# Kernel tuning notes

Hardware: AMD Instinct MI355X
Metric: run time of the kernel (lower is better)

The kernel has to match this reference:

```python
import jax, jax.numpy as jnp
import numpy as np

B, T, I, H, O = 64, 512, 64, 1024, 64
STEPS = 49 - 1  # output_len - 1 decode iterations


def _cell(x_t, h, c, Wih, Whh, b):
    # PyTorch LSTM gate order: i, f, g, o
    gates = x_t @ Wih.T + h @ Whh.T + b  # [B, 4H]
    i, f, g, o = jnp.split(gates, 4, axis=-1)
    i = jax.nn.sigmoid(i)
    f = jax.nn.sigmoid(f)
    g = jnp.tanh(g)
    o = jax.nn.sigmoid(o)
    c2 = f * c + i * g
    h2 = o * jnp.tanh(c2)
    return h2, c2


def setup_inputs() -> dict:
    key = jax.random.key(0)
    ks = jax.random.split(key, 12)
    s = 0.05
    return {
        "x": jax.random.normal(ks[0], (B, T, I), jnp.float32),
        "y0": jax.random.normal(ks[1], (B, I), jnp.float32),
        "Wih_e": jax.random.normal(ks[2], (4 * H, I), jnp.float32) * s,
        "Whh_e": jax.random.normal(ks[3], (4 * H, H), jnp.float32) * s,
        "bih_e": jax.random.normal(ks[4], (4 * H,), jnp.float32) * s,
        "bhh_e": jax.random.normal(ks[5], (4 * H,), jnp.float32) * s,
        "Wih_d": jax.random.normal(ks[6], (4 * H, I), jnp.float32) * s,
        "Whh_d": jax.random.normal(ks[7], (4 * H, H), jnp.float32) * s,
        "bih_d": jax.random.normal(ks[8], (4 * H,), jnp.float32) * s,
        "bhh_d": jax.random.normal(ks[9], (4 * H,), jnp.float32) * s,
        "Wfc": jax.random.normal(ks[10], (O, H), jnp.float32) * s,
        "bfc": jax.random.normal(ks[11], (O,), jnp.float32) * s,
    }


def reference(x, y0, Wih_e, Whh_e, bih_e, bhh_e, Wih_d, Whh_d, bih_d, bhh_d, Wfc, bfc):
    b = x.shape[0]
    h0 = jnp.zeros((b, Whh_e.shape[1]), x.dtype)
    c0 = h0

    # Encoder: scan over time (zero initial hidden, as in initHidden)
    be = bih_e + bhh_e

    def enc_step(carry, x_t):
        h, c = carry
        h, c = _cell(x_t, h, c, Wih_e, Whh_e, be)
        return (h, c), None

    (h, c), _ = jax.lax.scan(enc_step, (h0, c0), jnp.swapaxes(x, 0, 1))

    # Decoder: original loop never updates input_decoder -> constant y0 each step.
    bd = bih_d + bhh_d
    xin = y0 @ Wih_d.T + bd  # precompute constant input projection [B, 4H]

    def dec_step(carry, _):
        hd, cd = carry
        gates = xin + hd @ Whh_d.T
        i, f, g, o = jnp.split(gates, 4, axis=-1)
        i = jax.nn.sigmoid(i)
        f = jax.nn.sigmoid(f)
        g = jnp.tanh(g)
        o = jax.nn.sigmoid(o)
        c2 = f * cd + i * g
        h2 = o * jnp.tanh(c2)
        out = h2 @ Wfc.T + bfc  # [B, O]
        return (h2, c2), out

    _, ys = jax.lax.scan(dec_step, (h, c), None, length=STEPS)  # [STEPS, B, O]
    # torch.concat(total, dim=1): step-major along feature axis
    return jnp.swapaxes(ys, 0, 1).reshape(b, STEPS * ys.shape[-1])
```

## Files before the change

### kernel.cpp

```cpp
#include <hip/hip_runtime.h>
#include <hip/hip_fp16.h>

typedef _Float16 f16;
typedef _Float16 f16x8 __attribute__((ext_vector_type(8)));
typedef float f32x16 __attribute__((ext_vector_type(16)));

#define T_N 512
#define DSTEPS 48
#define TOTSTEPS 560
#define NWG 64

#define OFF_WHHE 0ull
#define SZ_WHH   (4096ull*1024*2)
#define OFF_WHHD (OFF_WHHE + SZ_WHH)
#define OFF_WIHE (OFF_WHHD + SZ_WHH)
#define SZ_WIH   (4096ull*64*2)
#define OFF_WIHD (OFF_WIHE + SZ_WIH)
#define OFF_WFC  (OFF_WIHD + SZ_WIH)
#define SZ_WFC   (64ull*1024*2)
#define OFF_XP   (OFF_WFC + SZ_WFC)
#define SZ_XP    (512ull*4096*2)
#define OFF_Y0   (OFF_XP + SZ_XP)
#define SZ_Y0    (4096ull*2)
#define OFF_BE   (OFF_Y0 + SZ_Y0)
#define OFF_BD   (OFF_BE + 4096ull*4)
#define OFF_FLG  (OFF_BD + 4096ull*4)
#define SZ_FLG   (561ull*256*4)
#define OFF_H    ((OFF_FLG + SZ_FLG + 255ull) & ~255ull)

__global__ void prologue(const float* __restrict__ x, const float* __restrict__ y0,
    const float* __restrict__ wihE, const float* __restrict__ whhE,
    const float* __restrict__ bihE, const float* __restrict__ bhhE,
    const float* __restrict__ wihD, const float* __restrict__ whhD,
    const float* __restrict__ bihD, const float* __restrict__ bhhD,
    const float* __restrict__ wfc, char* __restrict__ ws)
{
  const long long gid = (long long)blockIdx.x * 256 + threadIdx.x;
  const long long gsz = (long long)gridDim.x * 256;
  f16* whhEp = (f16*)(ws + OFF_WHHE);
  f16* whhDp = (f16*)(ws + OFF_WHHD);
  f16* wihEp = (f16*)(ws + OFF_WIHE);
  f16* wihDp = (f16*)(ws + OFF_WIHD);
  f16* wfcp  = (f16*)(ws + OFF_WFC);
  f16* xp    = (f16*)(ws + OFF_XP);
  f16* y0p   = (f16*)(ws + OFF_Y0);
  float* be  = (float*)(ws + OFF_BE);
  float* bd  = (float*)(ws + OFF_BD);

  for (long long idx = gid; idx < 4194304ll; idx += gsz) {
    int j = (int)idx & 7, l = (int)(idx >> 3) & 63, kk = (int)(idx >> 9) & 31;
    int i = (int)(idx >> 14) & 1, ks = (int)(idx >> 15) & 1, w = (int)(idx >> 16);
    int nl = i * 32 + (l & 31);
    int grow = (nl >> 4) * 1024 + w * 16 + (nl & 15);
    int k = ks * 512 + kk * 16 + ((l >> 5) << 3) + j;
    whhEp[idx] = (f16)whhE[(long long)grow * 1024 + k];
    whhDp[idx] = (f16)whhD[(long long)grow * 1024 + k];
  }
  for (long long idx = gid; idx < 262144ll; idx += gsz) {
    int j = (int)idx & 7, l = (int)(idx >> 3) & 63, kx = (int)(idx >> 9) & 1;
    int i = (int)(idx >> 10) & 1, ks = (int)(idx >> 11) & 1, w = (int)(idx >> 12);
    int nl = i * 32 + (l & 31);
    int grow = (nl >> 4) * 1024 + w * 16 + (nl & 15);
    int k = (ks * 2 + kx) * 16 + ((l >> 5) << 3) + j;
    wihEp[idx] = (f16)wihE[grow * 64 + k];
    wihDp[idx] = (f16)wihD[grow * 64 + k];
  }
  for (long long idx = gid; idx < 65536ll; idx += gsz) {
    int j = (int)idx & 7, l = (int)(idx >> 3) & 63, kk = (int)(idx >> 9) & 31;
    int i = (int)(idx >> 14) & 1, ks = (int)(idx >> 15) & 1;
    int o = i * 32 + (l & 31);
    int k = ks * 512 + kk * 16 + ((l >> 5) << 3) + j;
    wfcp[idx] = (f16)wfc[o * 1024 + k];
  }
  for (long long idx = gid; idx < 2097152ll; idx += gsz) {
    int kw = (int)idx & 15, b = (int)(idx >> 4) & 63, kkx = (int)(idx >> 10) & 3, t = (int)(idx >> 12);
    xp[idx] = (f16)x[(long long)b * 32768 + t * 64 + kkx * 16 + kw];
  }
  for (long long idx = gid; idx < 4096ll; idx += gsz) {
    int kw = (int)idx & 15, b = (int)(idx >> 4) & 63, kkx = (int)(idx >> 10) & 3;
    y0p[idx] = (f16)y0[b * 64 + kkx * 16 + kw];
  }
  for (long long idx = gid; idx < 4096ll; idx += gsz) {
    be[idx] = bihE[idx] + bhhE[idx];
    bd[idx] = bihD[idx] + bhhD[idx];
  }
}

__device__ __forceinline__ float sigf(float x) { return 1.0f / (1.0f + __expf(-x)); }
__device__ __forceinline__ float tanhfast(float x) {
  x = fminf(fmaxf(x, -15.f), 15.f);
  float e = __expf(2.0f * x);
  return (e - 1.0f) / (e + 1.0f);
}

#define MFMA(a,b,c) __builtin_amdgcn_mfma_f32_32x32x16_f16((a),(b),(c),0,0,0)

__launch_bounds__(256, 1)
__global__ void lstm_persist(char* __restrict__ ws, float* __restrict__ out,
                             const float* __restrict__ bfc)
{
  const int w    = blockIdx.x;
  const int tid  = threadIdx.x;
  const int lane = tid & 63;
  const int wave = tid >> 6;
  const int wm   = wave & 1;
  const int ks   = wave >> 1;

  const f16* whhEp = (const f16*)(ws + OFF_WHHE) + (size_t)w * 65536;
  const f16* whhDp = (const f16*)(ws + OFF_WHHD) + (size_t)w * 65536;
  const f16* wihEp = (const f16*)(ws + OFF_WIHE) + (size_t)w * 4096;
  const f16* wihDp = (const f16*)(ws + OFF_WIHD) + (size_t)w * 4096;
  const f16* wfcp  = (const f16*)(ws + OFF_WFC);
  const f16* xp    = (const f16*)(ws + OFF_XP);
  const f16* y0p   = (const f16*)(ws + OFF_Y0);
  const float* be  = (const float*)(ws + OFF_BE);
  const float* bd  = (const float*)(ws + OFF_BD);
  unsigned* flags  = (unsigned*)(ws + OFF_FLG);
  f16* hb          = (f16*)(ws + OFF_H);

  __shared__ float lds_g[2][64][66];
  __shared__ float bias_s[2][64];

  if (tid < 64) {
    int g4 = tid >> 4, u = tid & 15;
    bias_s[0][tid] = be[g4 * 1024 + w * 16 + u];
    bias_s[1][tid] = bd[g4 * 1024 + w * 16 + u];
  }

  const int aoff = (wm * 32 + (lane & 31)) * 16 + (lane >> 5) * 8;
  const int boff = lane * 8;
  const int bsel = tid >> 2;
  const int u0   = (tid & 3) * 4;

  f16x8 bf0[32], bf1[32];
#pragma unroll
  for (int kk = 0; kk < 32; ++kk) {
    bf0[kk] = *(const f16x8*)(whhEp + (size_t)ks * 32768 + kk * 512 + boff);
    bf1[kk] = *(const f16x8*)(whhEp + (size_t)ks * 32768 + 16384 + kk * 512 + boff);
  }

  float c0 = 0.f, c1 = 0.f, c2 = 0.f, c3 = 0.f;
  __syncthreads();

#pragma unroll 1
  for (int t = 0; t < TOTSTEPS; ++t) {
    const bool enc = (t < T_N);

    if (t == T_N) {
#pragma unroll
      for (int kk = 0; kk < 32; ++kk) {
        bf0[kk] = *(const f16x8*)(whhDp + (size_t)ks * 32768 + kk * 512 + boff);
        bf1[kk] = *(const f16x8*)(whhDp + (size_t)ks * 32768 + 16384 + kk * 512 + boff);
      }
    }

    const f16* xblk = enc ? (xp + (size_t)t * 4096) : y0p;
    const f16* wihp = enc ? wihEp : wihDp;
    f16x8 xa0 = *(const f16x8*)(xblk + (ks * 2 + 0) * 1024 + aoff);
    f16x8 xa1 = *(const f16x8*)(xblk + (ks * 2 + 1) * 1024 + aoff);
    f16x8 wf0 = *(const f16x8*)(wihp + ((ks * 2 + 0) * 2 + 0) * 512 + boff);
    f16x8 wf1 = *(const f16x8*)(wihp + ((ks * 2 + 0) * 2 + 1) * 512 + boff);
    f16x8 wf2 = *(const f16x8*)(wihp + ((ks * 2 + 1) * 2 + 0) * 512 + boff);
    f16x8 wf3 = *(const f16x8*)(wihp + ((ks * 2 + 1) * 2 + 1) * 512 + boff);

    if (t > 0) {
      const unsigned* fp0 = flags + (size_t)t * 256 + lane;
      int ok;
      do {
        unsigned v0 = __hip_atomic_load(fp0,       __ATOMIC_RELAXED, __HIP_MEMORY_SCOPE_AGENT);
        unsigned v1 = __hip_atomic_load(fp0 + 64,  __ATOMIC_RELAXED, __HIP_MEMORY_SCOPE_AGENT);
        unsigned v2 = __hip_atomic_load(fp0 + 128, __ATOMIC_RELAXED, __HIP_MEMORY_SCOPE_AGENT);
        unsigned v3 = __hip_atomic_load(fp0 + 192, __ATOMIC_RELAXED, __HIP_MEMORY_SCOPE_AGENT);
        ok = (v0 == 1u) & (v1 == 1u) & (v2 == 1u) & (v3 == 1u);
      } while (__syncthreads_and(ok) == 0);
    }

    f16x8 af[32];
    if (t > 0) {
      const f16* hblk = hb + (size_t)(t - 1) * 65536;
#pragma unroll
      for (int kk = 0; kk < 32; ++kk)
        af[kk] = *(const f16x8*)(hblk + (size_t)(ks * 32 + kk) * 1024 + aoff);
    }

    f32x16 acc0, acc1;
#pragma unroll
    for (int i = 0; i < 16; ++i) { acc0[i] = 0.f; acc1[i] = 0.f; }
    acc0 = MFMA(xa0, wf0, acc0); acc0 = MFMA(xa1, wf1, acc0);
    acc1 = MFMA(xa0, wf2, acc1); acc1 = MFMA(xa1, wf3, acc1);

    if (t > 0) {
#pragma unroll
      for (int kk = 0; kk < 32; ++kk) {
        acc0 = MFMA(af[kk], bf0[kk], acc0);
        acc1 = MFMA(af[kk], bf1[kk], acc1);
      }
    }

    {
      const int n0 = lane & 31;
      const int mb = wm * 32 + ((lane >> 5) << 2);
#pragma unroll
      for (int r = 0; r < 16; ++r) {
        const int m = mb + (r & 3) + ((r >> 2) << 3);
        lds_g[ks][n0][m]      = acc0[r];
        lds_g[ks][32 + n0][m] = acc1[r];
      }
    }
    __syncthreads();

    const float* bs = enc ? bias_s[0] : bias_s[1];
    union { unsigned long long u64; f16 h4[4]; } hu;
    float cc[4] = {c0, c1, c2, c3};
#pragma unroll
    for (int j = 0; j < 4; ++j) {
      const int u = u0 + j;
      float ig = lds_g[0][u][bsel]      + lds_g[1][u][bsel]      + bs[u];
      float fg = lds_g[0][16 + u][bsel] + lds_g[1][16 + u][bsel] + bs[16 + u];
      float gg = lds_g[0][32 + u][bsel] + lds_g[1][32 + u][bsel] + bs[32 + u];
      float og = lds_g[0][48 + u][bsel] + lds_g[1][48 + u][bsel] + bs[48 + u];
      float cn = sigf(fg) * cc[j] + sigf(ig) * tanhfast(gg);
      cc[j] = cn;
      hu.h4[j] = (f16)(sigf(og) * tanhfast(cn));
    }
    c0 = cc[0]; c1 = cc[1]; c2 = cc[2]; c3 = cc[3];

    {
      f16* dst = hb + (size_t)t * 65536 + (size_t)w * 1024 + bsel * 16 + u0;
      unsigned long long addr = (unsigned long long)(size_t)dst;
      asm volatile("global_store_dwordx2 %0, %1, off sc0 sc1" : : "v"(addr), "v"(hu.u64) : "memory");
    }
    asm volatile("s_waitcnt vmcnt(0)" ::: "memory");
    if (lane == 0) {
      unsigned* fa = flags + (size_t)(t + 1) * 256 + wave * 64 + w;
      unsigned long long addr = (unsigned long long)(size_t)fa;
      unsigned one = 1u;
      asm volatile("global_store_dword %0, %1, off sc0 sc1" : : "v"(addr), "v"(one) : "memory");
    }
  }

  if (w < DSTEPS) {
    const int s = T_N + 1 + w;
#pragma unroll
    for (int kk = 0; kk < 32; ++kk) {
      bf0[kk] = *(const f16x8*)(wfcp + (size_t)ks * 32768 + kk * 512 + boff);
      bf1[kk] = *(const f16x8*)(wfcp + (size_t)ks * 32768 + 16384 + kk * 512 + boff);
    }
    {
      const unsigned* fp0 = flags + (size_t)s * 256 + lane;
      int ok;
      do {
        unsigned v0 = __hip_atomic_load(fp0,       __ATOMIC_RELAXED, __HIP_MEMORY_SCOPE_AGENT);
        unsigned v1 = __hip_atomic_load(fp0 + 64,  __ATOMIC_RELAXED, __HIP_MEMORY_SCOPE_AGENT);
        unsigned v2 = __hip_atomic_load(fp0 + 128, __ATOMIC_RELAXED, __HIP_MEMORY_SCOPE_AGENT);
        unsigned v3 = __hip_atomic_load(fp0 + 192, __ATOMIC_RELAXED, __HIP_MEMORY_SCOPE_AGENT);
        ok = (v0 == 1u) & (v1 == 1u) & (v2 == 1u) & (v3 == 1u);
      } while (__syncthreads_and(ok) == 0);
    }
    const f16* hblk = hb + (size_t)(s - 1) * 65536;
    f16x8 af[32];
#pragma unroll
    for (int kk = 0; kk < 32; ++kk)
      af[kk] = *(const f16x8*)(hblk + (size_t)(ks * 32 + kk) * 1024 + aoff);

    f32x16 acc0, acc1;
#pragma unroll
    for (int i = 0; i < 16; ++i) { acc0[i] = 0.f; acc1[i] = 0.f; }
#pragma unroll
    for (int kk = 0; kk < 32; ++kk) {
      acc0 = MFMA(af[kk], bf0[kk], acc0);
      acc1 = MFMA(af[kk], bf1[kk], acc1);
    }
    {
      const int n0 = lane & 31;
      const int mb = wm * 32 + ((lane >> 5) << 2);
#pragma unroll
      for (int r = 0; r < 16; ++r) {
        const int m = mb + (r & 3) + ((r >> 2) << 3);
        lds_g[ks][n0][m]      = acc0[r];
        lds_g[ks][32 + n0][m] = acc1[r];
      }
    }
    __syncthreads();
    const int f0 = (tid & 3) * 16;
    float* op = out + (size_t)bsel * 3072 + w * 64 + f0;
#pragma unroll
    for (int c4 = 0; c4 < 4; ++c4) {
      float v4[4];
#pragma unroll
      for (int j = 0; j < 4; ++j) {
        const int f = f0 + c4 * 4 + j;
        v4[j] = lds_g[0][f][bsel] + lds_g[1][f][bsel] + bfc[f];
      }
      *(float4*)(op + c4 * 4) = make_float4(v4[0], v4[1], v4[2], v4[3]);
    }
  }
}

extern "C" void kernel_launch(void* const* d_in, const int* in_sizes, int n_in,
                              void* d_out, int out_size, void* d_ws, size_t ws_size,
                              hipStream_t stream) {
  const float* x    = (const float*)d_in[0];
  const float* y0   = (const float*)d_in[1];
  const float* wihE = (const float*)d_in[2];
  const float* whhE = (const float*)d_in[3];
  const float* bihE = (const float*)d_in[4];
  const float* bhhE = (const float*)d_in[5];
  const float* wihD = (const float*)d_in[6];
  const float* whhD = (const float*)d_in[7];
  const float* bihD = (const float*)d_in[8];
  const float* bhhD = (const float*)d_in[9];
  const float* wfc  = (const float*)d_in[10];
  const float* bfc  = (const float*)d_in[11];
  char* ws   = (char*)d_ws;
  float* out = (float*)d_out;

  prologue<<<256, 256, 0, stream>>>(x, y0, wihE, whhE, bihE, bhhE,
                                    wihD, whhD, bihD, bhhD, wfc, ws);
  lstm_persist<<<NWG, 256, 0, stream>>>(ws, out, bfc);
}
```

Baseline: 3.324 ms.

## Move recurrent weights to LDS, poll flags per wave, reduce gates with LDS atomics

Recurrent weight slices now sit in a 128KB shared-memory buffer and are read per step instead of being held in registers, which frees VGPRs. The block-wide __syncthreads_and flag poll becomes a per-wave __all poll on one flag per lane, so each wave starts its h loads and MFMAs as soon as its own K-slice producers are done. Gate partial sums from the two K-split waves are combined with LDS float atomic adds into one zeroed buffer, and each entry is reset after it is read. The trade-off is extra LDS bandwidth per step, atomic LDS traffic, an added barrier and very high LDS use.

```diff
diff --git a/kernel.cpp b/kernel.cpp
--- a/kernel.cpp
+++ b/kernel.cpp
@@ -118,9 +118,14 @@
   unsigned* flags  = (unsigned*)(ws + OFF_FLG);
   f16* hb          = (f16*)(ws + OFF_H);
 
-  __shared__ float lds_g[2][64][66];
+  __shared__ f16   whh_s[65536];
+  __shared__ float gred[64][67];
   __shared__ float bias_s[2][64];
 
+  for (int i = tid; i < 8192; i += 256)
+    ((float4*)whh_s)[i] = ((const float4*)whhEp)[i];
+  for (int i = tid; i < 64 * 67; i += 256)
+    (&gred[0][0])[i] = 0.f;
   if (tid < 64) {
     int g4 = tid >> 4, u = tid & 15;
     bias_s[0][tid] = be[g4 * 1024 + w * 16 + u];
@@ -131,13 +136,9 @@
   const int boff = lane * 8;
   const int bsel = tid >> 2;
   const int u0   = (tid & 3) * 4;
-
-  f16x8 bf0[32], bf1[32];
-#pragma unroll
-  for (int kk = 0; kk < 32; ++kk) {
-    bf0[kk] = *(const f16x8*)(whhEp + (size_t)ks * 32768 + kk * 512 + boff);
-    bf1[kk] = *(const f16x8*)(whhEp + (size_t)ks * 32768 + 16384 + kk * 512 + boff);
-  }
+  const f16* bfs = &whh_s[ks * 32768];
+
+  const unsigned* fpoll = flags + (2 * wm + (lane >> 5)) * 64 + 32 * ks + (lane & 31);
 
   float c0 = 0.f, c1 = 0.f, c2 = 0.f, c3 = 0.f;
   __syncthreads();
@@ -147,11 +148,9 @@
     const bool enc = (t < T_N);
 
     if (t == T_N) {
-#pragma unroll
-      for (int kk = 0; kk < 32; ++kk) {
-        bf0[kk] = *(const f16x8*)(whhDp + (size_t)ks * 32768 + kk * 512 + boff);
-        bf1[kk] = *(const f16x8*)(whhDp + (size_t)ks * 32768 + 16384 + kk * 512 + boff);
-      }
+      for (int i = tid; i < 8192; i += 256)
+        ((float4*)whh_s)[i] = ((const float4*)whhDp)[i];
+      __syncthreads();
     }
 
     const f16* xblk = enc ? (xp + (size_t)t * 4096) : y0p;
@@ -163,26 +162,6 @@
     f16x8 wf2 = *(const f16x8*)(wihp + ((ks * 2 + 1) * 2 + 0) * 512 + boff);
     f16x8 wf3 = *(const f16x8*)(wihp + ((ks * 2 + 1) * 2 + 1) * 512 + boff);
 
-    if (t > 0) {
-      const unsigned* fp0 = flags + (size_t)t * 256 + lane;
-      int ok;
-      do {
-        unsigned v0 = __hip_atomic_load(fp0,       __ATOMIC_RELAXED, __HIP_MEMORY_SCOPE_AGENT);
-        unsigned v1 = __hip_atomic_load(fp0 + 64,  __ATOMIC_RELAXED, __HIP_MEMORY_SCOPE_AGENT);
-        unsigned v2 = __hip_atomic_load(fp0 + 128, __ATOMIC_RELAXED, __HIP_MEMORY_SCOPE_AGENT);
-        unsigned v3 = __hip_atomic_load(fp0 + 192, __ATOMIC_RELAXED, __HIP_MEMORY_SCOPE_AGENT);
-        ok = (v0 == 1u) & (v1 == 1u) & (v2 == 1u) & (v3 == 1u);
-      } while (__syncthreads_and(ok) == 0);
-    }
-
-    f16x8 af[32];
-    if (t > 0) {
-      const f16* hblk = hb + (size_t)(t - 1) * 65536;
-#pragma unroll
-      for (int kk = 0; kk < 32; ++kk)
-        af[kk] = *(const f16x8*)(hblk + (size_t)(ks * 32 + kk) * 1024 + aoff);
-    }
-
     f32x16 acc0, acc1;
 #pragma unroll
     for (int i = 0; i < 16; ++i) { acc0[i] = 0.f; acc1[i] = 0.f; }
@@ -190,12 +169,29 @@
     acc1 = MFMA(xa0, wf2, acc1); acc1 = MFMA(xa1, wf3, acc1);
 
     if (t > 0) {
+      const unsigned* fp = fpoll + (size_t)t * 256;
+      unsigned v;
+      do {
+        v = __hip_atomic_load(fp, __ATOMIC_RELAXED, __HIP_MEMORY_SCOPE_AGENT);
+      } while (__all(v == 1u) == 0);
+      asm volatile("" ::: "memory");
+
+      const f16* hblk = hb + (size_t)(t - 1) * 65536;
+      f16x8 af[32];
+#pragma unroll
+      for (int kk = 0; kk < 32; ++kk)
+        af[kk] = *(const f16x8*)(hblk + (size_t)(ks * 32 + kk) * 1024 + aoff);
+
 #pragma unroll
       for (int kk = 0; kk < 32; ++kk) {
-        acc0 = MFMA(af[kk], bf0[kk], acc0);
-        acc1 = MFMA(af[kk], bf1[kk], acc1);
+        f16x8 b0 = *(const f16x8*)(bfs + kk * 512 + boff);
+        f16x8 b1 = *(const f16x8*)(bfs + 16384 + kk * 512 + boff);
+        acc0 = MFMA(af[kk], b0, acc0);
+        acc1 = MFMA(af[kk], b1, acc1);
       }
     }
+
+    __syncthreads();
 
     {
       const int n0 = lane & 31;
@@ -203,8 +199,8 @@
 #pragma unroll
       for (int r = 0; r < 16; ++r) {
         const int m = mb + (r & 3) + ((r >> 2) << 3);
-        lds_g[ks][n0][m]      = acc0[r];
-        lds_g[ks][32 + n0][m] = acc1[r];
+        (void)__hip_atomic_fetch_add(&gred[n0][m],      acc0[r], __ATOMIC_RELAXED, __HIP_MEMORY_SCOPE_WORKGROUP);
+        (void)__hip_atomic_fetch_add(&gred[32 + n0][m], acc1[r], __ATOMIC_RELAXED, __HIP_MEMORY_SCOPE_WORKGROUP);
       }
     }
     __syncthreads();
@@ -215,10 +211,12 @@
 #pragma unroll
     for (int j = 0; j < 4; ++j) {
       const int u = u0 + j;
-      float ig = lds_g[0][u][bsel]      + lds_g[1][u][bsel]      + bs[u];
-      float fg = lds_g[0][16 + u][bsel] + lds_g[1][16 + u][bsel] + bs[16 + u];
-      float gg = lds_g[0][32 + u][bsel] + lds_g[1][32 + u][bsel] + bs[32 + u];
-      float og = lds_g[0][48 + u][bsel] + lds_g[1][48 + u][bsel] + bs[48 + u];
+      float ig = gred[u][bsel]      + bs[u];
+      float fg = gred[16 + u][bsel] + bs[16 + u];
+      float gg = gred[32 + u][bsel] + bs[32 + u];
+      float og = gred[48 + u][bsel] + bs[48 + u];
+      gred[u][bsel] = 0.f; gred[16 + u][bsel] = 0.f;
+      gred[32 + u][bsel] = 0.f; gred[48 + u][bsel] = 0.f;
       float cn = sigf(fg) * cc[j] + sigf(ig) * tanhfast(gg);
       cc[j] = cn;
       hu.h4[j] = (f16)(sigf(og) * tanhfast(cn));
@@ -241,21 +239,17 @@
 
   if (w < DSTEPS) {
     const int s = T_N + 1 + w;
-#pragma unroll
-    for (int kk = 0; kk < 32; ++kk) {
-      bf0[kk] = *(const f16x8*)(wfcp + (size_t)ks * 32768 + kk * 512 + boff);
-      bf1[kk] = *(const f16x8*)(wfcp + (size_t)ks * 32768 + 16384 + kk * 512 + boff);
-    }
+    for (int i = tid; i < 8192; i += 256)
+      ((float4*)whh_s)[i] = ((const float4*)wfcp)[i];
+    __syncthreads();
+
     {
-      const unsigned* fp0 = flags + (size_t)s * 256 + lane;
-      int ok;
+      const unsigned* fp = fpoll + (size_t)s * 256;
+      unsigned v;
       do {
-        unsigned v0 = __hip_atomic_load(fp0,       __ATOMIC_RELAXED, __HIP_MEMORY_SCOPE_AGENT);
-        unsigned v1 = __hip_atomic_load(fp0 + 64,  __ATOMIC_RELAXED, __HIP_MEMORY_SCOPE_AGENT);
-        unsigned v2 = __hip_atomic_load(fp0 + 128, __ATOMIC_RELAXED, __HIP_MEMORY_SCOPE_AGENT);
-        unsigned v3 = __hip_atomic_load(fp0 + 192, __ATOMIC_RELAXED, __HIP_MEMORY_SCOPE_AGENT);
-        ok = (v0 == 1u) & (v1 == 1u) & (v2 == 1u) & (v3 == 1u);
-      } while (__syncthreads_and(ok) == 0);
+        v = __hip_atomic_load(fp, __ATOMIC_RELAXED, __HIP_MEMORY_SCOPE_AGENT);
+      } while (__all(v == 1u) == 0);
+      asm volatile("" ::: "memory");
     }
     const f16* hblk = hb + (size_t)(s - 1) * 65536;
     f16x8 af[32];
@@ -268,17 +262,20 @@
     for (int i = 0; i < 16; ++i) { acc0[i] = 0.f; acc1[i] = 0.f; }
 #pragma unroll
     for (int kk = 0; kk < 32; ++kk) {
-      acc0 = MFMA(af[kk], bf0[kk], acc0);
-      acc1 = MFMA(af[kk], bf1[kk], acc1);
-    }
+      f16x8 b0 = *(const f16x8*)(bfs + kk * 512 + boff);
+      f16x8 b1 = *(const f16x8*)(bfs + 16384 + kk * 512 + boff);
+      acc0 = MFMA(af[kk], b0, acc0);
+      acc1 = MFMA(af[kk], b1, acc1);
+    }
+    __syncthreads();
     {
       const int n0 = lane & 31;
       const int mb = wm * 32 + ((lane >> 5) << 2);
 #pragma unroll
       for (int r = 0; r < 16; ++r) {
         const int m = mb + (r & 3) + ((r >> 2) << 3);
-        lds_g[ks][n0][m]      = acc0[r];
-        lds_g[ks][32 + n0][m] = acc1[r];
+        (void)__hip_atomic_fetch_add(&gred[n0][m],      acc0[r], __ATOMIC_RELAXED, __HIP_MEMORY_SCOPE_WORKGROUP);
+        (void)__hip_atomic_fetch_add(&gred[32 + n0][m], acc1[r], __ATOMIC_RELAXED, __HIP_MEMORY_SCOPE_WORKGROUP);
       }
     }
     __syncthreads();
@@ -290,7 +287,7 @@
 #pragma unroll
       for (int j = 0; j < 4; ++j) {
         const int f = f0 + c4 * 4 + j;
-        v4[j] = lds_g[0][f][bsel] + lds_g[1][f][bsel] + bfc[f];
+        v4[j] = gred[f][bsel] + bfc[f];
       }
       *(float4*)(op + c4 * 4) = make_float4(v4[0], v4[1], v4[2], v4[3]);
     }
```

Result: slower. 9.710 ms (+192.1%).

## Poll only needed producer flags per wave and fold bias into accumulators

Applied to the files above, without the earlier changes.

Replaces the block-wide spin on all 256 step flags (with a __syncthreads_and every iteration) with a per-wave poll. Each wave checks only the flags of the producers whose h slices it reads, backs off with s_sleep, and fetches h right before its MFMAs. This aims to cut block-level barrier traffic and let waves start independently. Bias is now added into the ks==0 accumulators before the LDS write, which removes adds from the gate epilogue. An extra __syncthreads guards the reuse of the LDS buffer, and the correctness of the reduced flag subset depends on the tile-to-flag mapping.

```diff
diff --git a/kernel.cpp b/kernel.cpp
--- a/kernel.cpp
+++ b/kernel.cpp
@@ -131,6 +131,9 @@
   const int boff = lane * 8;
   const int bsel = tid >> 2;
   const int u0   = (tid & 3) * 4;
+  const int n0   = lane & 31;
+
+  const unsigned* fpoll = flags + (2 * wm + (lane >> 5)) * 64 + 32 * ks + (lane & 31);
 
   f16x8 bf0[32], bf1[32];
 #pragma unroll
@@ -163,26 +166,6 @@
     f16x8 wf2 = *(const f16x8*)(wihp + ((ks * 2 + 1) * 2 + 0) * 512 + boff);
     f16x8 wf3 = *(const f16x8*)(wihp + ((ks * 2 + 1) * 2 + 1) * 512 + boff);
 
-    if (t > 0) {
-      const unsigned* fp0 = flags + (size_t)t * 256 + lane;
-      int ok;
-      do {
-        unsigned v0 = __hip_atomic_load(fp0,       __ATOMIC_RELAXED, __HIP_MEMORY_SCOPE_AGENT);
-        unsigned v1 = __hip_atomic_load(fp0 + 64,  __ATOMIC_RELAXED, __HIP_MEMORY_SCOPE_AGENT);
-        unsigned v2 = __hip_atomic_load(fp0 + 128, __ATOMIC_RELAXED, __HIP_MEMORY_SCOPE_AGENT);
-        unsigned v3 = __hip_atomic_load(fp0 + 192, __ATOMIC_RELAXED, __HIP_MEMORY_SCOPE_AGENT);
-        ok = (v0 == 1u) & (v1 == 1u) & (v2 == 1u) & (v3 == 1u);
-      } while (__syncthreads_and(ok) == 0);
-    }
-
-    f16x8 af[32];
-    if (t > 0) {
-      const f16* hblk = hb + (size_t)(t - 1) * 65536;
-#pragma unroll
-      for (int kk = 0; kk < 32; ++kk)
-        af[kk] = *(const f16x8*)(hblk + (size_t)(ks * 32 + kk) * 1024 + aoff);
-    }
-
     f32x16 acc0, acc1;
 #pragma unroll
     for (int i = 0; i < 16; ++i) { acc0[i] = 0.f; acc1[i] = 0.f; }
@@ -190,6 +173,21 @@
     acc1 = MFMA(xa0, wf2, acc1); acc1 = MFMA(xa1, wf3, acc1);
 
     if (t > 0) {
+      const unsigned* fp = fpoll + (size_t)t * 256;
+      unsigned v;
+      do {
+        v = __hip_atomic_load(fp, __ATOMIC_RELAXED, __HIP_MEMORY_SCOPE_AGENT);
+        if (__all(v == 1u)) break;
+        __builtin_amdgcn_s_sleep(1);
+      } while (1);
+      asm volatile("" ::: "memory");
+
+      const f16* hblk = hb + (size_t)(t - 1) * 65536;
+      f16x8 af[32];
+#pragma unroll
+      for (int kk = 0; kk < 32; ++kk)
+        af[kk] = *(const f16x8*)(hblk + (size_t)(ks * 32 + kk) * 1024 + aoff);
+
 #pragma unroll
       for (int kk = 0; kk < 32; ++kk) {
         acc0 = MFMA(af[kk], bf0[kk], acc0);
@@ -197,8 +195,16 @@
       }
     }
 
+    if (ks == 0) {
+      const float* bs = enc ? bias_s[0] : bias_s[1];
+      float b0 = bs[n0], b1 = bs[32 + n0];
+#pragma unroll
+      for (int i = 0; i < 16; ++i) { acc0[i] += b0; acc1[i] += b1; }
+    }
+
+    __syncthreads();
+
     {
-      const int n0 = lane & 31;
       const int mb = wm * 32 + ((lane >> 5) << 2);
 #pragma unroll
       for (int r = 0; r < 16; ++r) {
@@ -209,16 +215,15 @@
     }
     __syncthreads();
 
-    const float* bs = enc ? bias_s[0] : bias_s[1];
     union { unsigned long long u64; f16 h4[4]; } hu;
     float cc[4] = {c0, c1, c2, c3};
 #pragma unroll
     for (int j = 0; j < 4; ++j) {
       const int u = u0 + j;
-      float ig = lds_g[0][u][bsel]      + lds_g[1][u][bsel]      + bs[u];
-      float fg = lds_g[0][16 + u][bsel] + lds_g[1][16 + u][bsel] + bs[16 + u];
-      float gg = lds_g[0][32 + u][bsel] + lds_g[1][32 + u][bsel] + bs[32 + u];
-      float og = lds_g[0][48 + u][bsel] + lds_g[1][48 + u][bsel] + bs[48 + u];
+      float ig = lds_g[0][u][bsel]      + lds_g[1][u][bsel];
+      float fg = lds_g[0][16 + u][bsel] + lds_g[1][16 + u][bsel];
+      float gg = lds_g[0][32 + u][bsel] + lds_g[1][32 + u][bsel];
+      float og = lds_g[0][48 + u][bsel] + lds_g[1][48 + u][bsel];
       float cn = sigf(fg) * cc[j] + sigf(ig) * tanhfast(gg);
       cc[j] = cn;
       hu.h4[j] = (f16)(sigf(og) * tanhfast(cn));
@@ -240,6 +245,7 @@
   }
 
   if (w < DSTEPS) {
+    __syncthreads();
     const int s = T_N + 1 + w;
 #pragma unroll
     for (int kk = 0; kk < 32; ++kk) {
@@ -247,16 +253,16 @@
       bf1[kk] = *(const f16x8*)(wfcp + (size_t)ks * 32768 + 16384 + kk * 512 + boff);
     }
     {
-      const unsigned* fp0 = flags + (size_t)s * 256 + lane;
-      int ok;
+      const unsigned* fp = fpoll + (size_t)s * 256;
+      unsigned v;
       do {
-        unsigned v0 = __hip_atomic_load(fp0,       __ATOMIC_RELAXED, __HIP_MEMORY_SCOPE_AGENT);
-        unsigned v1 = __hip_atomic_load(fp0 + 64,  __ATOMIC_RELAXED, __HIP_MEMORY_SCOPE_AGENT);
-        unsigned v2 = __hip_atomic_load(fp0 + 128, __ATOMIC_RELAXED, __HIP_MEMORY_SCOPE_AGENT);
-        unsigned v3 = __hip_atomic_load(fp0 + 192, __ATOMIC_RELAXED, __HIP_MEMORY_SCOPE_AGENT);
-        ok = (v0 == 1u) & (v1 == 1u) & (v2 == 1u) & (v3 == 1u);
-      } while (__syncthreads_and(ok) == 0);
-    }
+        v = __hip_atomic_load(fp, __ATOMIC_RELAXED, __HIP_MEMORY_SCOPE_AGENT);
+        if (__all(v == 1u)) break;
+        __builtin_amdgcn_s_sleep(1);
+      } while (1);
+      asm volatile("" ::: "memory");
+    }
+
     const f16* hblk = hb + (size_t)(s - 1) * 65536;
     f16x8 af[32];
 #pragma unroll
@@ -272,7 +278,6 @@
       acc1 = MFMA(af[kk], bf1[kk], acc1);
     }
     {
-      const int n0 = lane & 31;
       const int mb = wm * 32 + ((lane >> 5) << 2);
 #pragma unroll
       for (int r = 0; r < 16; ++r) {
```

New measurement: 6.196 ms. +86.4%, slower.
